# Optimization experiments

Hardware: AMD Instinct MI355X
Metric: run time of the kernel (lower is better)

The kernel has to match this reference:

```python
import jax, jax.numpy as jnp
import numpy as np

EMBED = 384
HEAD = 64


def setup_inputs() -> dict:
    key = jax.random.key(0)
    kx, kq, kk, kv = jax.random.split(key, 4)
    B, T = 4, 4096
    x = jax.random.normal(kx, (B, T, EMBED), dtype=jnp.float32)
    # torch Linear(384, 64, bias=False): weight (64, 384), y = x @ W.T.
    # Store pre-transposed as (EMBED, HEAD) so y = x @ W.
    s = 1.0 / np.sqrt(EMBED)  # kaiming-uniform-ish scale
    Wq = jax.random.uniform(kq, (EMBED, HEAD), jnp.float32, -s, s)
    Wk = jax.random.uniform(kk, (EMBED, HEAD), jnp.float32, -s, s)
    Wv = jax.random.uniform(kv, (EMBED, HEAD), jnp.float32, -s, s)
    return {"x": x, "Wq": Wq, "Wk": Wk, "Wv": Wv}


def reference(x, Wq, Wk, Wv):
    # q, k, v: [B, T, H]
    q = x @ Wq
    k = x @ Wk
    v = x @ Wv
    scale = k.shape[-1] ** (-0.5)
    scores = jnp.einsum("bth,bsh->bts", q, k) * scale  # [B, T, T]
    # Faithful to the original: tril, then mask anything equal to 0 with -inf
    # (this also masks exact zeros inside the causal region).
    tril = jnp.tril(scores)
    masked = jnp.where(tril == 0, -jnp.inf, tril)
    attn = jax.nn.softmax(masked, axis=-1)
    out = jnp.einsum("bts,bsh->bth", attn, v)  # [B, T, H]
    return out
```

## Files before the change

### kernel.cpp

```cpp
#include <hip/hip_runtime.h>
#include <hip/hip_bf16.h>
#include <stdint.h>


#define EMBED 384
#define HEAD  64
#define NB    4
#define NT    4096
#define NROWS (NB * NT)
#define NSPLIT 4

#define SCALE_Q 0.18033688011112042f

typedef short bf16x8 __attribute__((ext_vector_type(8)));
typedef float f32x4  __attribute__((ext_vector_type(4)));

__device__ __forceinline__ unsigned short bfround(float f) {
    union { float f; unsigned u; } v; v.f = f;
    return (unsigned short)((v.u + 0x8000u) >> 16);
}
__device__ __forceinline__ unsigned packbf(float lo, float hi) {
    union { float f; unsigned u; } a, b; a.f = lo; b.f = hi;
    return ((a.u + 0x8000u) >> 16) | ((b.u + 0x8000u) & 0xFFFF0000u);
}

__device__ __forceinline__ void pl_swap32(unsigned& a, unsigned& b) {
    asm("v_permlane32_swap_b32 %0, %1" : "+v"(a), "+v"(b));
}
__device__ __forceinline__ void pl_swap16(unsigned& a, unsigned& b) {
    asm("v_permlane16_swap_b32 %0, %1" : "+v"(a), "+v"(b));
}

__global__ __launch_bounds__(256)
void wprep_kernel(const float* __restrict__ Wq,
                  const float* __restrict__ Wk,
                  const float* __restrict__ Wv,
                  unsigned short* __restrict__ Wt)
{
    int idx = blockIdx.x * 256 + threadIdx.x;
    int k = idx / 192;
    int n = idx - k * 192;
    int sel = n >> 6, nc = n & 63;
    const float* wp = (sel == 0) ? Wq : ((sel == 1) ? Wk : Wv);
    Wt[n * EMBED + k] = bfround(wp[(size_t)k * HEAD + nc]);
}

__global__ __launch_bounds__(512)
void proj_kernel(const float* __restrict__ x,
                 const unsigned short* __restrict__ Wt,
                 unsigned short* __restrict__ Qo,
                 unsigned short* __restrict__ Ko,
                 unsigned short* __restrict__ Vto)
{
    __shared__ __attribute__((aligned(16))) unsigned short ws[2][192][128];
    __shared__ __attribute__((aligned(16))) unsigned short xs[2][64][128];
    unsigned short (*vbuf)[72] = (unsigned short (*)[72])&xs[1][0][0];

    const int t    = threadIdx.x;
    const int lane = t & 63;
    const int w    = t >> 6;
    const int quad = lane >> 4;
    const int l16  = lane & 15;
    const int wr   = w & 3;
    const int wc   = w >> 2;
    const int r0   = blockIdx.x * 64;

    const int xr  = t >> 5, xc4 = t & 31;
    const int xch = xc4 >> 1, xsub = (xc4 & 1) * 4;
    const int wrw = t >> 4, wcc = t & 15;

    f32x4 acc[6];
#pragma unroll
    for (int i = 0; i < 6; ++i) acc[i] = (f32x4){0.f, 0.f, 0.f, 0.f};

    float4 xv[4];
    uint4  wv[6];
#pragma unroll
    for (int i = 0; i < 4; ++i)
        xv[i] = *(const float4*)(x + (size_t)(r0 + xr + 16 * i) * EMBED + xc4 * 4);
#pragma unroll
    for (int i = 0; i < 6; ++i)
        wv[i] = *(const uint4*)(Wt + (size_t)(wrw + 32 * i) * EMBED + wcc * 8);

    int cur = 0;
#pragma unroll
    for (int ph = 0; ph < 3; ++ph) {
#pragma unroll
        for (int i = 0; i < 4; ++i) {
            int row = xr + 16 * i;
            uint2 pw; pw.x = packbf(xv[i].x, xv[i].y); pw.y = packbf(xv[i].z, xv[i].w);
            *(uint2*)&xs[cur][row][((xch ^ (row & 15)) << 3) + xsub] = pw;
        }
#pragma unroll
        for (int i = 0; i < 6; ++i) {
            int row = wrw + 32 * i;
            *(uint4*)&ws[cur][row][(wcc ^ (row & 15)) << 3] = wv[i];
        }
        __syncthreads();

        if (ph < 2) {
            const int k0 = (ph + 1) * 128;
#pragma unroll
            for (int i = 0; i < 4; ++i)
                xv[i] = *(const float4*)(x + (size_t)(r0 + xr + 16 * i) * EMBED + k0 + xc4 * 4);
#pragma unroll
            for (int i = 0; i < 6; ++i)
                wv[i] = *(const uint4*)(Wt + (size_t)(wrw + 32 * i) * EMBED + k0 + wcc * 8);
        }

#pragma unroll
        for (int s = 0; s < 4; ++s) {
            bf16x8 a = *(const bf16x8*)&xs[cur][wr * 16 + l16][((s * 4 + quad) ^ l16) << 3];
#pragma unroll
            for (int ng = 0; ng < 6; ++ng) {
                bf16x8 b = *(const bf16x8*)&ws[cur][wc * 96 + ng * 16 + l16][((s * 4 + quad) ^ l16) << 3];
                acc[ng] = __builtin_amdgcn_mfma_f32_16x16x32_bf16(a, b, acc[ng], 0, 0, 0);
            }
        }
        cur ^= 1;
    }
    __syncthreads();

#pragma unroll
    for (int ng = 0; ng < 6; ++ng) {
        int cg = wc * 96 + ng * 16 + l16;
#pragma unroll
        for (int r = 0; r < 4; ++r) {
            int row = r0 + wr * 16 + quad * 4 + r;
            float vv = acc[ng][r];
            if (cg < 64) {
                Qo[(size_t)row * HEAD + cg] = bfround(vv * SCALE_Q);
            } else if (cg < 128) {
                Ko[(size_t)row * HEAD + (cg - 64)] = bfround(vv);
            } else {
                vbuf[cg - 128][wr * 16 + quad * 4 + r] = bfround(vv);
            }
        }
    }
    __syncthreads();
    {
        const int batch = r0 >> 12;
        const int s0 = r0 & (NT - 1);
        const int d = t >> 3, c = t & 7;
        *(uint4*)(Vto + ((size_t)(batch * HEAD + d)) * NT + s0 + c * 8) =
            *(const uint4*)&vbuf[d][c * 8];
    }
}

__global__ __launch_bounds__(256, 4)
void attn_kernel(const unsigned short* __restrict__ Qi,
                 const unsigned short* __restrict__ Ki,
                 const unsigned short* __restrict__ Vti,
                 float* __restrict__ opart,
                 float* __restrict__ lpart)
{
    __shared__ __attribute__((aligned(16))) unsigned short Kt[2][64][64];
    __shared__ __attribute__((aligned(16))) unsigned short Vs[2][64][64];

    const int t    = threadIdx.x;
    const int w    = t >> 6;
    const int lane = t & 63;
    const int quad = lane >> 4;
    const int l16  = lane & 15;

    const int u = blockIdx.x;
    const int g = u >> 4;
    const int m = (g < 32) ? (63 - g) : (g - 32);
    const int sp = (u >> 2) & 3;
    const int batch = u & 3;
    const int ntiles = (m >= sp) ? (((m - sp) >> 2) + 1) : 0;
    const int q0 = m * 64 + w * 16;

    const unsigned short* Kbg = Ki  + (size_t)batch * NT * HEAD;
    const unsigned short* Vbg = Vti + (size_t)batch * HEAD * NT;

    bf16x8 bq0, bq1;
    {
        const unsigned short* qp = Qi + (size_t)(batch * NT + q0 + l16) * HEAD + quad * 8;
        bq0 = *(const bf16x8*)(qp);
        bq1 = *(const bf16x8*)(qp + 32);
    }

    f32x4 o[4];
#pragma unroll
    for (int i = 0; i < 4; ++i) o[i] = (f32x4){0.f, 0.f, 0.f, 0.f};
    float rs = 0.f;

    const int srow0 = t >> 3, sc = t & 7;
    const int srow1 = (t + 256) >> 3;
    const int scc0 = sc ^ (srow0 & 7);
    const int scc1 = sc ^ (srow1 & 7);
    const int sw = l16 & 7;

    uint4 kr0, kr1, vr0, vr1;
    if (ntiles > 0) {
        const int kt = sp;
        kr0 = *(const uint4*)(Kbg + (size_t)(kt * 64 + srow0) * HEAD + sc * 8);
        kr1 = *(const uint4*)(Kbg + (size_t)(kt * 64 + srow1) * HEAD + sc * 8);
        vr0 = *(const uint4*)(Vbg + (size_t)srow0 * NT + kt * 64 + sc * 8);
        vr1 = *(const uint4*)(Vbg + (size_t)srow1 * NT + kt * 64 + sc * 8);
    }

    int cur = 0;
    for (int j = 0; j < ntiles; ++j) {
        const int kt = sp + 4 * j;
        *(uint4*)&Kt[cur][srow0][scc0 * 8] = kr0;
        *(uint4*)&Kt[cur][srow1][scc1 * 8] = kr1;
        *(uint4*)&Vs[cur][srow0][scc0 * 8] = vr0;
        *(uint4*)&Vs[cur][srow1][scc1 * 8] = vr1;
        __syncthreads();

        if (j + 1 < ntiles) {
            const int ktn = kt + 4;
            kr0 = *(const uint4*)(Kbg + (size_t)(ktn * 64 + srow0) * HEAD + sc * 8);
            kr1 = *(const uint4*)(Kbg + (size_t)(ktn * 64 + srow1) * HEAD + sc * 8);
            vr0 = *(const uint4*)(Vbg + (size_t)srow0 * NT + ktn * 64 + sc * 8);
            vr1 = *(const uint4*)(Vbg + (size_t)srow1 * NT + ktn * 64 + sc * 8);
        }

        const bool diag = (kt == m);
        uint2 pw[4];
#pragma unroll
        for (int ts = 0; ts < 4; ++ts) {
            bf16x8 ak0 = *(const bf16x8*)&Kt[cur][ts * 16 + l16][(quad ^ sw) * 8];
            bf16x8 ak1 = *(const bf16x8*)&Kt[cur][ts * 16 + l16][((4 + quad) ^ sw) * 8];
            f32x4 z = (f32x4){0.f, 0.f, 0.f, 0.f};
            z = __builtin_amdgcn_mfma_f32_16x16x32_bf16(ak0, bq0, z, 0, 0, 0);
            z = __builtin_amdgcn_mfma_f32_16x16x32_bf16(ak1, bq1, z, 0, 0, 0);
            float p[4];
#pragma unroll
            for (int r = 0; r < 4; ++r) {
                float pv = __builtin_amdgcn_exp2f(z[r]);
                if (diag) {
                    int sg = kt * 64 + ts * 16 + quad * 4 + r;
                    pv = (sg > q0 + l16) ? 0.f : pv;
                }
                p[r] = pv;
            }
            rs += (p[0] + p[1]) + (p[2] + p[3]);
            pw[ts].x = packbf(p[0], p[1]);
            pw[ts].y = packbf(p[2], p[3]);
        }

        unsigned a0 = pw[0].x, c0 = pw[0].y, b0 = pw[1].x, d0 = pw[1].y;
        pl_swap32(a0, b0); pl_swap32(c0, d0);
        pl_swap16(a0, b0); pl_swap16(c0, d0);
        unsigned a1 = pw[2].x, c1 = pw[2].y, b1 = pw[3].x, d1 = pw[3].y;
        pl_swap32(a1, b1); pl_swap32(c1, d1);
        pl_swap16(a1, b1); pl_swap16(c1, d1);
        union { unsigned u[4]; bf16x8 v; } ua0, ua1;
        ua0.u[0] = a0; ua0.u[1] = c0; ua0.u[2] = b0; ua0.u[3] = d0;
        ua1.u[0] = a1; ua1.u[1] = c1; ua1.u[2] = b1; ua1.u[3] = d1;
        const bf16x8 ap0 = ua0.v;
        const bf16x8 ap1 = ua1.v;

#pragma unroll
        for (int nd = 0; nd < 4; ++nd) {
            bf16x8 av0 = *(const bf16x8*)&Vs[cur][nd * 16 + l16][(quad ^ sw) * 8];
            bf16x8 av1 = *(const bf16x8*)&Vs[cur][nd * 16 + l16][((4 + quad) ^ sw) * 8];
            o[nd] = __builtin_amdgcn_mfma_f32_16x16x32_bf16(ap0, av0, o[nd], 0, 0, 0);
            o[nd] = __builtin_amdgcn_mfma_f32_16x16x32_bf16(ap1, av1, o[nd], 0, 0, 0);
        }
        cur ^= 1;
    }

    rs += __shfl_xor(rs, 16, 64);
    rs += __shfl_xor(rs, 32, 64);
    if (quad == 0)
        lpart[(size_t)sp * NROWS + batch * NT + q0 + l16] = rs;
    float* ob = opart + (size_t)sp * NROWS * HEAD;
#pragma unroll
    for (int r = 0; r < 4; ++r) {
        size_t off = (size_t)(batch * NT + q0 + quad * 4 + r) * HEAD;
#pragma unroll
        for (int nd = 0; nd < 4; ++nd)
            ob[off + nd * 16 + l16] = o[nd][r];
    }
}

__global__ __launch_bounds__(256)
void combine_kernel(const float* __restrict__ opart,
                    const float* __restrict__ lpart,
                    float* __restrict__ out)
{
    int gid = blockIdx.x * 256 + threadIdx.x;
    int row = gid >> 4;
    int d4  = (gid & 15) * 4;
    const size_t st = (size_t)NROWS * HEAD;
    const float* p0 = opart + (size_t)row * HEAD + d4;
    f32x4 a = *(const f32x4*)(p0);
    f32x4 b = *(const f32x4*)(p0 + st);
    f32x4 c = *(const f32x4*)(p0 + 2 * st);
    f32x4 d = *(const f32x4*)(p0 + 3 * st);
    float inv = 1.0f / (lpart[row] + lpart[NROWS + row] +
                        lpart[2 * NROWS + row] + lpart[3 * NROWS + row]);
    f32x4 res = (a + b) + (c + d);
    res[0] *= inv; res[1] *= inv; res[2] *= inv; res[3] *= inv;
    *(f32x4*)(out + (size_t)row * HEAD + d4) = res;
}

extern "C" void kernel_launch(void* const* d_in, const int* in_sizes, int n_in,
                              void* d_out, int out_size, void* d_ws, size_t ws_size,
                              hipStream_t stream)
{
    const float* x  = (const float*)d_in[0];
    const float* Wq = (const float*)d_in[1];
    const float* Wk = (const float*)d_in[2];
    const float* Wv = (const float*)d_in[3];
    float* out = (float*)d_out;

    unsigned short* Qw  = (unsigned short*)d_ws;
    unsigned short* Kw  = Qw + (size_t)NROWS * HEAD;
    unsigned short* Vtw = Kw + (size_t)NROWS * HEAD;
    unsigned short* Wtw = Vtw + (size_t)NROWS * HEAD;
    float* opart = (float*)(Wtw + (size_t)192 * EMBED);
    float* lpart = opart + (size_t)NSPLIT * NROWS * HEAD;

    wprep_kernel<<<(192 * EMBED) / 256, 256, 0, stream>>>(Wq, Wk, Wv, Wtw);
    proj_kernel<<<256, 512, 0, stream>>>(x, Wtw, Qw, Kw, Vtw);
    attn_kernel<<<1024, 256, 0, stream>>>(Qw, Kw, Vtw, opart, lpart);
    combine_kernel<<<NROWS * 16 / 256, 256, 0, stream>>>(opart, lpart, out);
}
```

Baseline: 105.8 us.

## Split key tile across two waves per query group and reduce via LDS

The attention block grows to 512 threads, with each pair of waves sharing a 16-row query group and each wave handling half of the 64-key tile. The partial outputs and row sums are then combined through shared memory before being written out. This halves per-wave MFMA and exp work and doubles the waves available to hide latency, at the cost of an extra LDS reduction and barrier at the end. It also replaces the manual bf16 rounding with the hardware packed convert instruction.

```diff
diff --git a/kernel.cpp b/kernel.cpp
--- a/kernel.cpp
+++ b/kernel.cpp
@@ -22,6 +22,11 @@
 __device__ __forceinline__ unsigned packbf(float lo, float hi) {
     union { float f; unsigned u; } a, b; a.f = lo; b.f = hi;
     return ((a.u + 0x8000u) >> 16) | ((b.u + 0x8000u) & 0xFFFF0000u);
+}
+__device__ __forceinline__ unsigned cvtpk(float lo, float hi) {
+    unsigned r;
+    asm("v_cvt_pk_bf16_f32 %0, %1, %2" : "=v"(r) : "v"(lo), "v"(hi));
+    return r;
 }
 
 __device__ __forceinline__ void pl_swap32(unsigned& a, unsigned& b) {
@@ -147,7 +152,7 @@
     }
 }
 
-__global__ __launch_bounds__(256, 4)
+__global__ __launch_bounds__(512, 8)
 void attn_kernel(const unsigned short* __restrict__ Qi,
                  const unsigned short* __restrict__ Ki,
                  const unsigned short* __restrict__ Vti,
@@ -162,6 +167,8 @@
     const int lane = t & 63;
     const int quad = lane >> 4;
     const int l16  = lane & 15;
+    const int qg   = w >> 1;
+    const int sh   = w & 1;
 
     const int u = blockIdx.x;
     const int g = u >> 4;
@@ -169,7 +176,7 @@
     const int sp = (u >> 2) & 3;
     const int batch = u & 3;
     const int ntiles = (m >= sp) ? (((m - sp) >> 2) + 1) : 0;
-    const int q0 = m * 64 + w * 16;
+    const int q0 = m * 64 + qg * 16;
 
     const unsigned short* Kbg = Ki  + (size_t)batch * NT * HEAD;
     const unsigned short* Vbg = Vti + (size_t)batch * HEAD * NT;
@@ -186,42 +193,34 @@
     for (int i = 0; i < 4; ++i) o[i] = (f32x4){0.f, 0.f, 0.f, 0.f};
     float rs = 0.f;
 
-    const int srow0 = t >> 3, sc = t & 7;
-    const int srow1 = (t + 256) >> 3;
-    const int scc0 = sc ^ (srow0 & 7);
-    const int scc1 = sc ^ (srow1 & 7);
-    const int sw = l16 & 7;
-
-    uint4 kr0, kr1, vr0, vr1;
+    const int srow = t >> 3, sc = t & 7;
+    const int scc  = sc ^ (srow & 7);
+    const int sw   = l16 & 7;
+
+    uint4 kr, vr;
     if (ntiles > 0) {
-        const int kt = sp;
-        kr0 = *(const uint4*)(Kbg + (size_t)(kt * 64 + srow0) * HEAD + sc * 8);
-        kr1 = *(const uint4*)(Kbg + (size_t)(kt * 64 + srow1) * HEAD + sc * 8);
-        vr0 = *(const uint4*)(Vbg + (size_t)srow0 * NT + kt * 64 + sc * 8);
-        vr1 = *(const uint4*)(Vbg + (size_t)srow1 * NT + kt * 64 + sc * 8);
+        kr = *(const uint4*)(Kbg + (size_t)(sp * 64 + srow) * HEAD + sc * 8);
+        vr = *(const uint4*)(Vbg + (size_t)srow * NT + sp * 64 + sc * 8);
     }
 
     int cur = 0;
     for (int j = 0; j < ntiles; ++j) {
         const int kt = sp + 4 * j;
-        *(uint4*)&Kt[cur][srow0][scc0 * 8] = kr0;
-        *(uint4*)&Kt[cur][srow1][scc1 * 8] = kr1;
-        *(uint4*)&Vs[cur][srow0][scc0 * 8] = vr0;
-        *(uint4*)&Vs[cur][srow1][scc1 * 8] = vr1;
+        *(uint4*)&Kt[cur][srow][scc * 8] = kr;
+        *(uint4*)&Vs[cur][srow][scc * 8] = vr;
         __syncthreads();
 
         if (j + 1 < ntiles) {
             const int ktn = kt + 4;
-            kr0 = *(const uint4*)(Kbg + (size_t)(ktn * 64 + srow0) * HEAD + sc * 8);
-            kr1 = *(const uint4*)(Kbg + (size_t)(ktn * 64 + srow1) * HEAD + sc * 8);
-            vr0 = *(const uint4*)(Vbg + (size_t)srow0 * NT + ktn * 64 + sc * 8);
-            vr1 = *(const uint4*)(Vbg + (size_t)srow1 * NT + ktn * 64 + sc * 8);
+            kr = *(const uint4*)(Kbg + (size_t)(ktn * 64 + srow) * HEAD + sc * 8);
+            vr = *(const uint4*)(Vbg + (size_t)srow * NT + ktn * 64 + sc * 8);
         }
 
         const bool diag = (kt == m);
-        uint2 pw[4];
-#pragma unroll
-        for (int ts = 0; ts < 4; ++ts) {
+        uint2 pw[2];
+#pragma unroll
+        for (int tsl = 0; tsl < 2; ++tsl) {
+            const int ts = sh * 2 + tsl;
             bf16x8 ak0 = *(const bf16x8*)&Kt[cur][ts * 16 + l16][(quad ^ sw) * 8];
             bf16x8 ak1 = *(const bf16x8*)&Kt[cur][ts * 16 + l16][((4 + quad) ^ sw) * 8];
             f32x4 z = (f32x4){0.f, 0.f, 0.f, 0.f};
@@ -238,43 +237,53 @@
                 p[r] = pv;
             }
             rs += (p[0] + p[1]) + (p[2] + p[3]);
-            pw[ts].x = packbf(p[0], p[1]);
-            pw[ts].y = packbf(p[2], p[3]);
+            pw[tsl].x = cvtpk(p[0], p[1]);
+            pw[tsl].y = cvtpk(p[2], p[3]);
         }
 
         unsigned a0 = pw[0].x, c0 = pw[0].y, b0 = pw[1].x, d0 = pw[1].y;
         pl_swap32(a0, b0); pl_swap32(c0, d0);
         pl_swap16(a0, b0); pl_swap16(c0, d0);
-        unsigned a1 = pw[2].x, c1 = pw[2].y, b1 = pw[3].x, d1 = pw[3].y;
-        pl_swap32(a1, b1); pl_swap32(c1, d1);
-        pl_swap16(a1, b1); pl_swap16(c1, d1);
-        union { unsigned u[4]; bf16x8 v; } ua0, ua1;
-        ua0.u[0] = a0; ua0.u[1] = c0; ua0.u[2] = b0; ua0.u[3] = d0;
-        ua1.u[0] = a1; ua1.u[1] = c1; ua1.u[2] = b1; ua1.u[3] = d1;
-        const bf16x8 ap0 = ua0.v;
-        const bf16x8 ap1 = ua1.v;
+        union { unsigned uu[4]; bf16x8 v; } ua;
+        ua.uu[0] = a0; ua.uu[1] = c0; ua.uu[2] = b0; ua.uu[3] = d0;
+        const bf16x8 ap = ua.v;
 
 #pragma unroll
         for (int nd = 0; nd < 4; ++nd) {
-            bf16x8 av0 = *(const bf16x8*)&Vs[cur][nd * 16 + l16][(quad ^ sw) * 8];
-            bf16x8 av1 = *(const bf16x8*)&Vs[cur][nd * 16 + l16][((4 + quad) ^ sw) * 8];
-            o[nd] = __builtin_amdgcn_mfma_f32_16x16x32_bf16(ap0, av0, o[nd], 0, 0, 0);
-            o[nd] = __builtin_amdgcn_mfma_f32_16x16x32_bf16(ap1, av1, o[nd], 0, 0, 0);
+            bf16x8 av = *(const bf16x8*)&Vs[cur][nd * 16 + l16][((4 * sh + quad) ^ sw) * 8];
+            o[nd] = __builtin_amdgcn_mfma_f32_16x16x32_bf16(ap, av, o[nd], 0, 0, 0);
         }
         cur ^= 1;
     }
 
     rs += __shfl_xor(rs, 16, 64);
     rs += __shfl_xor(rs, 32, 64);
-    if (quad == 0)
-        lpart[(size_t)sp * NROWS + batch * NT + q0 + l16] = rs;
-    float* ob = opart + (size_t)sp * NROWS * HEAD;
-#pragma unroll
-    for (int r = 0; r < 4; ++r) {
-        size_t off = (size_t)(batch * NT + q0 + quad * 4 + r) * HEAD;
+
+    __syncthreads();
+    float* osc = (float*)&Kt[0][0][0];
+    float* rsc = (float*)&Vs[0][0][0];
+    if (sh == 1) {
 #pragma unroll
         for (int nd = 0; nd < 4; ++nd)
-            ob[off + nd * 16 + l16] = o[nd][r];
+#pragma unroll
+            for (int r = 0; r < 4; ++r)
+                osc[(qg * 16 + quad * 4 + r) * 64 + nd * 16 + l16] = o[nd][r];
+        if (quad == 0) rsc[qg * 16 + l16] = rs;
+    }
+    __syncthreads();
+    if (sh == 0) {
+        rs += rsc[qg * 16 + l16];
+        if (quad == 0)
+            lpart[(size_t)sp * NROWS + batch * NT + q0 + l16] = rs;
+        float* ob = opart + (size_t)sp * NROWS * HEAD;
+#pragma unroll
+        for (int r = 0; r < 4; ++r) {
+            size_t off = (size_t)(batch * NT + q0 + quad * 4 + r) * HEAD;
+#pragma unroll
+            for (int nd = 0; nd < 4; ++nd)
+                ob[off + nd * 16 + l16] =
+                    o[nd][r] + osc[(qg * 16 + quad * 4 + r) * 64 + nd * 16 + l16];
+        }
     }
 }
 
@@ -318,6 +327,6 @@
 
     wprep_kernel<<<(192 * EMBED) / 256, 256, 0, stream>>>(Wq, Wk, Wv, Wtw);
     proj_kernel<<<256, 512, 0, stream>>>(x, Wtw, Qw, Kw, Vtw);
-    attn_kernel<<<1024, 256, 0, stream>>>(Qw, Kw, Vtw, opart, lpart);
+    attn_kernel<<<1024, 512, 0, stream>>>(Qw, Kw, Vtw, opart, lpart);
     combine_kernel<<<NROWS * 16 / 256, 256, 0, stream>>>(opart, lpart, out);
 }
```

Result: no change. 103.8 us (-1.9%).
